# Kernel optimization log

Hardware: AMD Instinct MI355X
Metric: run time of the kernel (lower is better)

## Reference

```python
import jax, jax.numpy as jnp
import numpy as np

INPUT_DIM = 256
OUTPUT_DIM = 256
COND_DIM = 128
HIDDEN = 128
BATCH = 512


def setup_inputs() -> dict:
    key = jax.random.key(0)
    ks = jax.random.split(key, 8)
    IO = INPUT_DIM * OUTPUT_DIM
    x = jax.random.normal(ks[0], (BATCH, INPUT_DIM), dtype=jnp.float32)
    cond = jax.random.normal(ks[1], (BATCH, COND_DIM), dtype=jnp.float32)
    base_weight = jax.random.normal(ks[2], (INPUT_DIM, OUTPUT_DIM), dtype=jnp.float32) * 0.01
    base_bias = jnp.zeros((OUTPUT_DIM,), dtype=jnp.float32)
    # hypernet: Linear(cond_dim, hidden) -> ReLU -> Linear(hidden, I*O + O)
    w1 = jax.random.normal(ks[3], (COND_DIM, HIDDEN), dtype=jnp.float32) * (1.0 / np.sqrt(COND_DIM))
    b1 = jnp.zeros((HIDDEN,), dtype=jnp.float32)
    w2 = jax.random.normal(ks[4], (HIDDEN, IO + OUTPUT_DIM), dtype=jnp.float32) * (1.0 / np.sqrt(HIDDEN))
    b2 = jnp.zeros((IO + OUTPUT_DIM,), dtype=jnp.float32)
    return {"x": x, "cond": cond, "base_weight": base_weight, "base_bias": base_bias,
            "w1": w1, "b1": b1, "w2": w2, "b2": b2}


def reference(x, cond, base_weight, base_bias, w1, b1, w2, b2):
    B = x.shape[0]
    IO = INPUT_DIM * OUTPUT_DIM
    # hypernet MLP producing per-sample weight/bias deltas
    h = jax.nn.relu(cond @ w1 + b1)                      # [B, hidden]
    dyn = h @ w2 + b2                                    # [B, I*O + O]
    weight_delta = dyn[:, :IO].reshape(B, INPUT_DIM, OUTPUT_DIM)
    bias_delta = dyn[:, IO:]                             # [B, O]
    W = base_weight[None, :, :] + weight_delta           # [B, I, O]
    b = base_bias[None, :] + bias_delta                  # [B, O]
    out = jnp.einsum('bi,bio->bo', x, W) + b             # per-sample GEMV
    return out
```

## Files before the change

### kernel.cpp

```cpp
#include <hip/hip_runtime.h>
#include <hip/hip_bf16.h>
#include <stdint.h>

#define BATCH    512
#define IN_DIM   256
#define OUT_DIM  256
#define COND_DIM 128
#define HIDDEN   128
#define W2_COLS  65792
#define H_STRIDE 132
#define NCHUNKS  34
#define OUT_ELEMS (BATCH * OUT_DIM)
#define WS_NEEDED ((size_t)NCHUNKS * OUT_ELEMS * 2)

typedef __attribute__((ext_vector_type(8))) short bf16x8;
typedef __attribute__((ext_vector_type(4))) float f32x4;

__device__ float g_h[BATCH * H_STRIDE];

static __device__ __forceinline__ unsigned short f2bf(float f) {
    union { float f; unsigned int u; } v; v.f = f;
    unsigned int r = v.u + 0x7FFFu + ((v.u >> 16) & 1u);
    return (unsigned short)(r >> 16);
}
static __device__ __forceinline__ unsigned int pack2(float a, float b) {
    return (unsigned int)f2bf(a) | ((unsigned int)f2bf(b) << 16);
}
static __device__ __forceinline__ float bf2f(unsigned short u) {
    union { unsigned int u; float f; } v; v.u = ((unsigned int)u) << 16;
    return v.f;
}

__global__ void hyper_h_kernel(const float* __restrict__ cond,
                               const float* __restrict__ w1,
                               const float* __restrict__ b1) {
    __shared__ float c[COND_DIM];
    int b = blockIdx.x;
    int k = threadIdx.x;
    c[k] = cond[b * COND_DIM + k];
    __syncthreads();
    float acc = b1[k];
    #pragma unroll 8
    for (int i = 0; i < COND_DIM; ++i)
        acc += c[i] * w1[i * HIDDEN + k];
    g_h[b * H_STRIDE + k] = fmaxf(acc, 0.0f);
    if (k < 4) g_h[b * H_STRIDE + 128 + k] = 1.0f;
}

__global__ __launch_bounds__(256, 4)
void hyper_main_kernel(const float* __restrict__ x,
                       const float* __restrict__ base_weight,
                       const float* __restrict__ w2,
                       const float* __restrict__ b2,
                       unsigned short* __restrict__ ws) {
    __shared__ __align__(16) unsigned short A_lds[2][4096];
    __shared__ __align__(16) unsigned short B_lds[2][4096];

    const int bx    = blockIdx.x;
    const int chunk = bx >> 5;
    const int rem   = bx & 31;
    const int b0    = (rem >> 2) * 64;
    const int o0    = (rem & 3) * 64;
    const bool is_bias = (chunk == 33);
    const int nstage   = (chunk < 32) ? 16 : (chunk == 32 ? 8 : 2);
    const int p_base   = chunk * 4;

    const int t    = threadIdx.x;
    const int lane = t & 63;
    const int wave = t >> 6;
    const int wm   = wave >> 1, wn = wave & 1;
    const int qg   = lane >> 4, ncol = lane & 15;

    const int ab = t >> 2, aq = t & 3;
    const int np = (t & 31) * 2, kq = t >> 5;

    f32x4 acc[2][2];
    #pragma unroll
    for (int i = 0; i < 2; ++i)
        #pragma unroll
        for (int j = 0; j < 2; ++j) acc[i][j] = (f32x4){0.f, 0.f, 0.f, 0.f};

    float4 pa[4]; float phs; float2 pbv[8];

    auto issue = [&](int s) {
        if (!is_bias) {
            int p  = p_base + (s >> 2);
            int i0 = (s & 3) * 64;
            const float* pb = (p < 128) ? (w2 + (size_t)p * W2_COLS)
                                        : (p == 128 ? b2 : base_weight);
            phs = g_h[(b0 + ab) * H_STRIDE + p];
            const float4* xs = (const float4*)(x + (size_t)(b0 + ab) * IN_DIM + i0 + aq * 16);
            #pragma unroll
            for (int q = 0; q < 4; ++q) pa[q] = xs[q];
            const float* bb = pb + (size_t)(i0 + kq * 8) * OUT_DIM + o0 + np;
            #pragma unroll
            for (int j = 0; j < 8; ++j)
                pbv[j] = *(const float2*)(bb + (size_t)j * OUT_DIM);
        } else {
            int k0 = s * 64;
            phs = 1.0f;
            const float4* hs = (const float4*)(g_h + (size_t)(b0 + ab) * H_STRIDE + k0 + aq * 16);
            #pragma unroll
            for (int q = 0; q < 4; ++q) pa[q] = hs[q];
            const float* bb = w2 + 65536 + (size_t)(k0 + kq * 8) * W2_COLS + o0 + np;
            #pragma unroll
            for (int j = 0; j < 8; ++j)
                pbv[j] = *(const float2*)(bb + (size_t)j * W2_COLS);
        }
    };
    auto commit = [&](int buf) {
        uint4 u0, u1;
        u0.x = pack2(pa[0].x * phs, pa[0].y * phs);
        u0.y = pack2(pa[0].z * phs, pa[0].w * phs);
        u0.z = pack2(pa[1].x * phs, pa[1].y * phs);
        u0.w = pack2(pa[1].z * phs, pa[1].w * phs);
        u1.x = pack2(pa[2].x * phs, pa[2].y * phs);
        u1.y = pack2(pa[2].z * phs, pa[2].w * phs);
        u1.z = pack2(pa[3].x * phs, pa[3].y * phs);
        u1.w = pack2(pa[3].z * phs, pa[3].w * phs);
        int sw = ab & 7;
        *(uint4*)&A_lds[buf][(ab * 8 + ((aq * 2)     ^ sw)) * 8] = u0;
        *(uint4*)&A_lds[buf][(ab * 8 + ((aq * 2 + 1) ^ sw)) * 8] = u1;
        uint4 v0, v1;
        v0.x = pack2(pbv[0].x, pbv[1].x); v0.y = pack2(pbv[2].x, pbv[3].x);
        v0.z = pack2(pbv[4].x, pbv[5].x); v0.w = pack2(pbv[6].x, pbv[7].x);
        v1.x = pack2(pbv[0].y, pbv[1].y); v1.y = pack2(pbv[2].y, pbv[3].y);
        v1.z = pack2(pbv[4].y, pbv[5].y); v1.w = pack2(pbv[6].y, pbv[7].y);
        *(uint4*)&B_lds[buf][( np      * 8 + (kq ^ ( np      & 7))) * 8] = v0;
        *(uint4*)&B_lds[buf][((np + 1) * 8 + (kq ^ ((np + 1) & 7))) * 8] = v1;
    };

    issue(0);
    commit(0);
    __syncthreads();

    for (int s = 0; s < nstage; ++s) {
        const int cur = s & 1;
        if (s + 1 < nstage) issue(s + 1);

        #pragma unroll
        for (int ks = 0; ks < 2; ++ks) {
            const int kg = ks * 4 + qg;
            bf16x8 af[2], bfr[2];
            #pragma unroll
            for (int mf = 0; mf < 2; ++mf) {
                int m = wm * 32 + mf * 16 + ncol;
                af[mf] = *(const bf16x8*)&A_lds[cur][(m * 8 + (kg ^ (m & 7))) * 8];
            }
            #pragma unroll
            for (int nf = 0; nf < 2; ++nf) {
                int n = wn * 32 + nf * 16 + ncol;
                bfr[nf] = *(const bf16x8*)&B_lds[cur][(n * 8 + (kg ^ (n & 7))) * 8];
            }
            #pragma unroll
            for (int mf = 0; mf < 2; ++mf)
                #pragma unroll
                for (int nf = 0; nf < 2; ++nf)
                    acc[mf][nf] = __builtin_amdgcn_mfma_f32_16x16x32_bf16(
                        af[mf], bfr[nf], acc[mf][nf], 0, 0, 0);
        }

        if (s + 1 < nstage) commit(1 - cur);
        __syncthreads();
    }

    unsigned short* slice = ws + (size_t)chunk * OUT_ELEMS;
    #pragma unroll
    for (int mf = 0; mf < 2; ++mf)
        #pragma unroll
        for (int nf = 0; nf < 2; ++nf)
            #pragma unroll
            for (int reg = 0; reg < 4; ++reg) {
                int row = b0 + wm * 32 + mf * 16 + qg * 4 + reg;
                int col = o0 + wn * 32 + nf * 16 + ncol;
                slice[(size_t)row * OUT_DIM + col] = f2bf(acc[mf][nf][reg]);
            }
}

__global__ void hyper_reduce_kernel(const unsigned short* __restrict__ ws,
                                    const float* __restrict__ base_bias,
                                    const float* __restrict__ b2,
                                    float* __restrict__ out) {
    int i = blockIdx.x * 256 + threadIdx.x;
    int o = (i & 63) * 4;
    float4 bb = *(const float4*)(base_bias + o);
    float4 c2 = *(const float4*)(b2 + 65536 + o);
    float4 a;
    a.x = bb.x + c2.x; a.y = bb.y + c2.y; a.z = bb.z + c2.z; a.w = bb.w + c2.w;
    #pragma unroll
    for (int c = 0; c < NCHUNKS; ++c) {
        ushort4 v = *(const ushort4*)(ws + (size_t)c * OUT_ELEMS + (size_t)i * 4);
        a.x += bf2f(v.x); a.y += bf2f(v.y); a.z += bf2f(v.z); a.w += bf2f(v.w);
    }
    ((float4*)out)[i] = a;
}

extern "C" void kernel_launch(void* const* d_in, const int* in_sizes, int n_in,
                              void* d_out, int out_size, void* d_ws, size_t ws_size,
                              hipStream_t stream) {
    const float* x           = (const float*)d_in[0];
    const float* cond        = (const float*)d_in[1];
    const float* base_weight = (const float*)d_in[2];
    const float* base_bias   = (const float*)d_in[3];
    const float* w1          = (const float*)d_in[4];
    const float* b1          = (const float*)d_in[5];
    const float* w2          = (const float*)d_in[6];
    const float* b2          = (const float*)d_in[7];
    float* out = (float*)d_out;
    unsigned short* ws = (unsigned short*)d_ws;

    hyper_h_kernel<<<BATCH, COND_DIM, 0, stream>>>(cond, w1, b1);
    hyper_main_kernel<<<NCHUNKS * 32, 256, 0, stream>>>(x, base_weight, w2, b2, ws);
    hyper_reduce_kernel<<<OUT_ELEMS / 4 / 256, 256, 0, stream>>>(ws, base_bias, b2, out);
}
```

Measured before the change: 130.2 us.

## Pre-transpose weights to bf16 planes and use direct-to-LDS loads in GEMM

A new prep kernel converts all w2 planes, b2 and base_weight to bf16 in a transposed [o][i] layout. The same kernel converts x and h to bf16 and computes the hidden layer. The main GEMM then keeps x fragments in registers, streams weight tiles into LDS with global_load_lds, and applies the per-plane h scaling after each plane's MFMA partial. This removes per-block fp32 loads and the conversion and repacking that were repeated for every batch tile. In exchange it adds an extra full read and write pass over the ~34 MB weight tensor every call, plus workspace traffic.

```diff
diff --git a/kernel.cpp b/kernel.cpp
--- a/kernel.cpp
+++ b/kernel.cpp
@@ -9,14 +9,17 @@
 #define HIDDEN   128
 #define W2_COLS  65792
 #define H_STRIDE 132
+#define PLANE_SZ 65536
 #define NCHUNKS  34
 #define OUT_ELEMS (BATCH * OUT_DIM)
-#define WS_NEEDED ((size_t)NCHUNKS * OUT_ELEMS * 2)
+#define SLICE_OFF ((size_t)131 * PLANE_SZ)
 
 typedef __attribute__((ext_vector_type(8))) short bf16x8;
 typedef __attribute__((ext_vector_type(4))) float f32x4;
 
-__device__ float g_h[BATCH * H_STRIDE];
+__device__ float          g_h[BATCH * H_STRIDE + 8];
+__device__ unsigned short g_hbf[BATCH * HIDDEN];
+__device__ unsigned short g_xbf[BATCH * IN_DIM];
 
 static __device__ __forceinline__ unsigned short f2bf(float f) {
     union { float f; unsigned int u; } v; v.f = f;
@@ -31,153 +34,199 @@
     return v.f;
 }
 
-__global__ void hyper_h_kernel(const float* __restrict__ cond,
-                               const float* __restrict__ w1,
-                               const float* __restrict__ b1) {
-    __shared__ float c[COND_DIM];
-    int b = blockIdx.x;
-    int k = threadIdx.x;
-    c[k] = cond[b * COND_DIM + k];
-    __syncthreads();
-    float acc = b1[k];
-    #pragma unroll 8
-    for (int i = 0; i < COND_DIM; ++i)
-        acc += c[i] * w1[i * HIDDEN + k];
-    g_h[b * H_STRIDE + k] = fmaxf(acc, 0.0f);
-    if (k < 4) g_h[b * H_STRIDE + 128 + k] = 1.0f;
-}
-
-__global__ __launch_bounds__(256, 4)
-void hyper_main_kernel(const float* __restrict__ x,
+__global__ __launch_bounds__(256)
+void hyper_prep_kernel(const float* __restrict__ x,
+                       const float* __restrict__ cond,
                        const float* __restrict__ base_weight,
+                       const float* __restrict__ w1,
+                       const float* __restrict__ b1,
                        const float* __restrict__ w2,
                        const float* __restrict__ b2,
-                       unsigned short* __restrict__ ws) {
-    __shared__ __align__(16) unsigned short A_lds[2][4096];
-    __shared__ __align__(16) unsigned short B_lds[2][4096];
+                       unsigned short* __restrict__ wt) {
+    const int bx = blockIdx.x;
+    const int t  = threadIdx.x;
+    if (bx < 2088) {
+        int p, it, ot; const float* src; int rstride;
+        if (bx < 2080) {
+            p = bx >> 4; int sub = bx & 15; it = sub >> 2; ot = sub & 3;
+            src = (p < 128) ? (w2 + (size_t)p * W2_COLS) : (p == 128 ? b2 : base_weight);
+            rstride = OUT_DIM;
+        } else {
+            p = 130; int sub = bx - 2080; it = sub >> 2; ot = sub & 3;
+            src = w2 + 65536; rstride = W2_COLS;
+        }
+        int o  = ot * 64 + (t & 63);
+        int i0 = it * 64 + (t >> 6) * 16;
+        unsigned int vv[8];
+        #pragma unroll
+        for (int r = 0; r < 8; ++r) {
+            float a = src[(size_t)(i0 + 2 * r)     * rstride + o];
+            float b = src[(size_t)(i0 + 2 * r + 1) * rstride + o];
+            vv[r] = pack2(a, b);
+        }
+        unsigned int* dst = (unsigned int*)(wt + (size_t)p * PLANE_SZ + (size_t)o * 256 + i0);
+        *(uint4*)dst       = *(uint4*)&vv[0];
+        *(uint4*)(dst + 4) = *(uint4*)&vv[4];
+    } else if (bx < 2104) {
+        int base = (bx - 2088) * 8192 + t * 32;
+        #pragma unroll
+        for (int g = 0; g < 4; ++g) {
+            const float4* s4 = (const float4*)(x + base + g * 8);
+            float4 a = s4[0], b = s4[1];
+            unsigned int vv[4] = { pack2(a.x, a.y), pack2(a.z, a.w),
+                                   pack2(b.x, b.y), pack2(b.z, b.w) };
+            *(uint4*)(g_xbf + base + g * 8) = *(uint4*)vv;
+        }
+    } else {
+        __shared__ float c[2][COND_DIM];
+        int bb = t >> 7, k = t & 127;
+        int b  = (bx - 2104) * 2 + bb;
+        c[bb][k] = cond[b * COND_DIM + k];
+        __syncthreads();
+        float acc = b1[k];
+        #pragma unroll 8
+        for (int i = 0; i < COND_DIM; ++i)
+            acc += c[bb][i] * w1[i * HIDDEN + k];
+        acc = fmaxf(acc, 0.0f);
+        g_h[b * H_STRIDE + k] = acc;
+        g_hbf[b * HIDDEN + k] = f2bf(acc);
+        if (k < 4) g_h[b * H_STRIDE + 128 + k] = 1.0f;
+    }
+}
+
+template<int NSLABS>
+static __device__ __forceinline__ void run_gemm(
+    int nplanes, int p0, const unsigned short* asrc, int astride,
+    const unsigned short* __restrict__ wt, unsigned short* __restrict__ slices,
+    int chunk, int b0, int o0, int t,
+    unsigned short (*B_lds)[64 * 64], float* h_s)
+{
+    const int lane = t & 63, wave = t >> 6;
+    const int wm = wave >> 1, wn = wave & 1;
+    const int qg = lane >> 4, ncol = lane & 15;
+
+    const int drow = lane >> 3;
+    const int dcol = ((lane & 7) ^ drow) * 8;
+
+    bf16x8 xf[NSLABS][2][2];
+    #pragma unroll
+    for (int sl = 0; sl < NSLABS; ++sl)
+        #pragma unroll
+        for (int ks = 0; ks < 2; ++ks)
+            #pragma unroll
+            for (int mf = 0; mf < 2; ++mf)
+                xf[sl][ks][mf] = *(const bf16x8*)(asrc
+                    + (size_t)(b0 + wm * 32 + mf * 16 + ncol) * astride
+                    + sl * 64 + ks * 32 + qg * 8);
+
+    f32x4 acc[2][2] = {};
+    f32x4 pacc[2][2];
+    float hv[2][4];
+
+    auto dmaB = [&](int plane, int i0, int buf) {
+        const unsigned short* gp = wt + (size_t)plane * PLANE_SZ
+            + (size_t)(o0 + wave * 16 + drow) * 256 + i0 + dcol;
+        __builtin_amdgcn_global_load_lds(
+            (const __attribute__((address_space(1))) unsigned int*)gp,
+            (__attribute__((address_space(3))) unsigned int*)&B_lds[buf][wave * 16 * 64],
+            16, 0, 0);
+        __builtin_amdgcn_global_load_lds(
+            (const __attribute__((address_space(1))) unsigned int*)(gp + 8 * 256),
+            (__attribute__((address_space(3))) unsigned int*)&B_lds[buf][(wave * 16 + 8) * 64],
+            16, 0, 0);
+    };
+
+    dmaB(p0, 0, 0);
+    __syncthreads();
+
+    for (int pl = 0; pl < nplanes; ++pl) {
+        #pragma unroll
+        for (int sl = 0; sl < NSLABS; ++sl) {
+            const int buf = sl & 1;
+            if (sl + 1 < NSLABS)          dmaB(p0 + pl,     (sl + 1) * 64, buf ^ 1);
+            else if (pl + 1 < nplanes)    dmaB(p0 + pl + 1, 0,             buf ^ 1);
+
+            if (sl == 0) {
+                #pragma unroll
+                for (int mf = 0; mf < 2; ++mf)
+                    #pragma unroll
+                    for (int r = 0; r < 4; ++r)
+                        hv[mf][r] = h_s[(wm * 32 + mf * 16 + qg * 4 + r) * 4 + pl];
+                #pragma unroll
+                for (int a = 0; a < 2; ++a)
+                    #pragma unroll
+                    for (int bq = 0; bq < 2; ++bq)
+                        pacc[a][bq] = (f32x4){0.f, 0.f, 0.f, 0.f};
+            }
+
+            #pragma unroll
+            for (int ks = 0; ks < 2; ++ks) {
+                bf16x8 bfr[2];
+                #pragma unroll
+                for (int nf = 0; nf < 2; ++nf) {
+                    int n = wn * 32 + nf * 16 + ncol;
+                    bfr[nf] = *(const bf16x8*)&B_lds[buf][(n * 8 + ((ks * 4 + qg) ^ (n & 7))) * 8];
+                }
+                #pragma unroll
+                for (int mf = 0; mf < 2; ++mf)
+                    #pragma unroll
+                    for (int nf = 0; nf < 2; ++nf)
+                        pacc[mf][nf] = __builtin_amdgcn_mfma_f32_16x16x32_bf16(
+                            xf[sl][ks][mf], bfr[nf], pacc[mf][nf], 0, 0, 0);
+            }
+
+            if (sl == NSLABS - 1) {
+                #pragma unroll
+                for (int mf = 0; mf < 2; ++mf)
+                    #pragma unroll
+                    for (int nf = 0; nf < 2; ++nf)
+                        #pragma unroll
+                        for (int r = 0; r < 4; ++r)
+                            acc[mf][nf][r] += hv[mf][r] * pacc[mf][nf][r];
+            }
+            __syncthreads();
+        }
+    }
+
+    unsigned short* slice = slices + (size_t)chunk * OUT_ELEMS;
+    #pragma unroll
+    for (int mf = 0; mf < 2; ++mf)
+        #pragma unroll
+        for (int nf = 0; nf < 2; ++nf)
+            #pragma unroll
+            for (int r = 0; r < 4; ++r) {
+                int row = b0 + wm * 32 + mf * 16 + qg * 4 + r;
+                int col = o0 + wn * 32 + nf * 16 + ncol;
+                slice[(size_t)row * OUT_DIM + col] = f2bf(acc[mf][nf][r]);
+            }
+}
+
+__global__ __launch_bounds__(256, 3)
+void hyper_main_kernel(const unsigned short* __restrict__ wt,
+                       unsigned short* __restrict__ slices) {
+    __shared__ __align__(16) unsigned short B_lds[2][64 * 64];
+    __shared__ float h_s[256];
 
     const int bx    = blockIdx.x;
     const int chunk = bx >> 5;
     const int rem   = bx & 31;
     const int b0    = (rem >> 2) * 64;
     const int o0    = (rem & 3) * 64;
-    const bool is_bias = (chunk == 33);
-    const int nstage   = (chunk < 32) ? 16 : (chunk == 32 ? 8 : 2);
-    const int p_base   = chunk * 4;
-
-    const int t    = threadIdx.x;
-    const int lane = t & 63;
-    const int wave = t >> 6;
-    const int wm   = wave >> 1, wn = wave & 1;
-    const int qg   = lane >> 4, ncol = lane & 15;
-
-    const int ab = t >> 2, aq = t & 3;
-    const int np = (t & 31) * 2, kq = t >> 5;
-
-    f32x4 acc[2][2];
-    #pragma unroll
-    for (int i = 0; i < 2; ++i)
-        #pragma unroll
-        for (int j = 0; j < 2; ++j) acc[i][j] = (f32x4){0.f, 0.f, 0.f, 0.f};
-
-    float4 pa[4]; float phs; float2 pbv[8];
-
-    auto issue = [&](int s) {
-        if (!is_bias) {
-            int p  = p_base + (s >> 2);
-            int i0 = (s & 3) * 64;
-            const float* pb = (p < 128) ? (w2 + (size_t)p * W2_COLS)
-                                        : (p == 128 ? b2 : base_weight);
-            phs = g_h[(b0 + ab) * H_STRIDE + p];
-            const float4* xs = (const float4*)(x + (size_t)(b0 + ab) * IN_DIM + i0 + aq * 16);
-            #pragma unroll
-            for (int q = 0; q < 4; ++q) pa[q] = xs[q];
-            const float* bb = pb + (size_t)(i0 + kq * 8) * OUT_DIM + o0 + np;
-            #pragma unroll
-            for (int j = 0; j < 8; ++j)
-                pbv[j] = *(const float2*)(bb + (size_t)j * OUT_DIM);
-        } else {
-            int k0 = s * 64;
-            phs = 1.0f;
-            const float4* hs = (const float4*)(g_h + (size_t)(b0 + ab) * H_STRIDE + k0 + aq * 16);
-            #pragma unroll
-            for (int q = 0; q < 4; ++q) pa[q] = hs[q];
-            const float* bb = w2 + 65536 + (size_t)(k0 + kq * 8) * W2_COLS + o0 + np;
-            #pragma unroll
-            for (int j = 0; j < 8; ++j)
-                pbv[j] = *(const float2*)(bb + (size_t)j * W2_COLS);
-        }
-    };
-    auto commit = [&](int buf) {
-        uint4 u0, u1;
-        u0.x = pack2(pa[0].x * phs, pa[0].y * phs);
-        u0.y = pack2(pa[0].z * phs, pa[0].w * phs);
-        u0.z = pack2(pa[1].x * phs, pa[1].y * phs);
-        u0.w = pack2(pa[1].z * phs, pa[1].w * phs);
-        u1.x = pack2(pa[2].x * phs, pa[2].y * phs);
-        u1.y = pack2(pa[2].z * phs, pa[2].w * phs);
-        u1.z = pack2(pa[3].x * phs, pa[3].y * phs);
-        u1.w = pack2(pa[3].z * phs, pa[3].w * phs);
-        int sw = ab & 7;
-        *(uint4*)&A_lds[buf][(ab * 8 + ((aq * 2)     ^ sw)) * 8] = u0;
-        *(uint4*)&A_lds[buf][(ab * 8 + ((aq * 2 + 1) ^ sw)) * 8] = u1;
-        uint4 v0, v1;
-        v0.x = pack2(pbv[0].x, pbv[1].x); v0.y = pack2(pbv[2].x, pbv[3].x);
-        v0.z = pack2(pbv[4].x, pbv[5].x); v0.w = pack2(pbv[6].x, pbv[7].x);
-        v1.x = pack2(pbv[0].y, pbv[1].y); v1.y = pack2(pbv[2].y, pbv[3].y);
-        v1.z = pack2(pbv[4].y, pbv[5].y); v1.w = pack2(pbv[6].y, pbv[7].y);
-        *(uint4*)&B_lds[buf][( np      * 8 + (kq ^ ( np      & 7))) * 8] = v0;
-        *(uint4*)&B_lds[buf][((np + 1) * 8 + (kq ^ ((np + 1) & 7))) * 8] = v1;
-    };
-
-    issue(0);
-    commit(0);
-    __syncthreads();
-
-    for (int s = 0; s < nstage; ++s) {
-        const int cur = s & 1;
-        if (s + 1 < nstage) issue(s + 1);
-
-        #pragma unroll
-        for (int ks = 0; ks < 2; ++ks) {
-            const int kg = ks * 4 + qg;
-            bf16x8 af[2], bfr[2];
-            #pragma unroll
-            for (int mf = 0; mf < 2; ++mf) {
-                int m = wm * 32 + mf * 16 + ncol;
-                af[mf] = *(const bf16x8*)&A_lds[cur][(m * 8 + (kg ^ (m & 7))) * 8];
-            }
-            #pragma unroll
-            for (int nf = 0; nf < 2; ++nf) {
-                int n = wn * 32 + nf * 16 + ncol;
-                bfr[nf] = *(const bf16x8*)&B_lds[cur][(n * 8 + (kg ^ (n & 7))) * 8];
-            }
-            #pragma unroll
-            for (int mf = 0; mf < 2; ++mf)
-                #pragma unroll
-                for (int nf = 0; nf < 2; ++nf)
-                    acc[mf][nf] = __builtin_amdgcn_mfma_f32_16x16x32_bf16(
-                        af[mf], bfr[nf], acc[mf][nf], 0, 0, 0);
-        }
-
-        if (s + 1 < nstage) commit(1 - cur);
-        __syncthreads();
-    }
-
-    unsigned short* slice = ws + (size_t)chunk * OUT_ELEMS;
-    #pragma unroll
-    for (int mf = 0; mf < 2; ++mf)
-        #pragma unroll
-        for (int nf = 0; nf < 2; ++nf)
-            #pragma unroll
-            for (int reg = 0; reg < 4; ++reg) {
-                int row = b0 + wm * 32 + mf * 16 + qg * 4 + reg;
-                int col = o0 + wn * 32 + nf * 16 + ncol;
-                slice[(size_t)row * OUT_DIM + col] = f2bf(acc[mf][nf][reg]);
-            }
-}
-
-__global__ void hyper_reduce_kernel(const unsigned short* __restrict__ ws,
+    const int t     = threadIdx.x;
+
+    int p0 = (chunk < 32) ? chunk * 4 : (chunk == 32 ? 128 : 130);
+
+    h_s[t] = g_h[(b0 + (t >> 2)) * H_STRIDE + p0 + (t & 3)];
+
+    if (chunk < 33)
+        run_gemm<4>(chunk < 32 ? 4 : 2, p0, g_xbf, IN_DIM,
+                    wt, slices, chunk, b0, o0, t, B_lds, h_s);
+    else
+        run_gemm<2>(1, p0, g_hbf, HIDDEN,
+                    wt, slices, chunk, b0, o0, t, B_lds, h_s);
+}
+
+__global__ void hyper_reduce_kernel(const unsigned short* __restrict__ slices,
                                     const float* __restrict__ base_bias,
                                     const float* __restrict__ b2,
                                     float* __restrict__ out) {
@@ -189,7 +238,7 @@
     a.x = bb.x + c2.x; a.y = bb.y + c2.y; a.z = bb.z + c2.z; a.w = bb.w + c2.w;
     #pragma unroll
     for (int c = 0; c < NCHUNKS; ++c) {
-        ushort4 v = *(const ushort4*)(ws + (size_t)c * OUT_ELEMS + (size_t)i * 4);
+        ushort4 v = *(const ushort4*)(slices + (size_t)c * OUT_ELEMS + (size_t)i * 4);
         a.x += bf2f(v.x); a.y += bf2f(v.y); a.z += bf2f(v.z); a.w += bf2f(v.w);
     }
     ((float4*)out)[i] = a;
@@ -209,7 +258,7 @@
     float* out = (float*)d_out;
     unsigned short* ws = (unsigned short*)d_ws;
 
-    hyper_h_kernel<<<BATCH, COND_DIM, 0, stream>>>(cond, w1, b1);
-    hyper_main_kernel<<<NCHUNKS * 32, 256, 0, stream>>>(x, base_weight, w2, b2, ws);
-    hyper_reduce_kernel<<<OUT_ELEMS / 4 / 256, 256, 0, stream>>>(ws, base_bias, b2, out);
-}
+    hyper_prep_kernel<<<2360, 256, 0, stream>>>(x, cond, base_weight, w1, b1, w2, b2, ws);
+    hyper_main_kernel<<<NCHUNKS * 32, 256, 0, stream>>>(ws, ws + SLICE_OFF);
+    hyper_reduce_kernel<<<OUT_ELEMS / 4 / 256, 256, 0, stream>>>(ws + SLICE_OFF, base_bias, b2, out);
+}
```

Measured after the change: 123.8 us. 1.05x faster.
